# Kernel optimization log

Hardware: AMD Instinct MI355X
Metric: run time of the kernel (lower is better)

## Reference

```python
import jax, jax.numpy as jnp
import numpy as np

B, F, W, H, D = 128, 1024, 32, 64, 64  # batch, n_features, window_size, hidden_state, output_dim


def setup_inputs() -> dict:
    key = jax.random.key(0)
    ks = jax.random.split(key, 8)
    sd = 0.05
    return {
        "x": jax.random.normal(ks[0], (B, F, W), jnp.float32),
        # dense_state: Dense(output_dim) on concat([cell, hidden]) -> [2H, D]
        "W_state": jax.random.normal(ks[1], (2 * H, D), jnp.float32) * sd,
        "b_state": jnp.zeros((D,), jnp.float32),
        # dense: Dense(output_dim, use_bias=False) on input last dim W -> [W, D]
        "W_in": jax.random.normal(ks[2], (W, D), jnp.float32) * sd,
        # Dense(1) scoring layer (shared; original re-creates it each call)
        "w_attn": jax.random.normal(ks[3], (D, 1), jnp.float32) * sd,
        "b_attn": jnp.zeros((1,), jnp.float32),
        # Keras LSTMCell params, gate order i, f, g(c~), o
        "Wx": jax.random.normal(ks[4], (F, 4 * H), jnp.float32) * sd,
        "Wh": jax.random.normal(ks[5], (H, 4 * H), jnp.float32) * sd,
        "b_lstm": jnp.zeros((4 * H,), jnp.float32),
    }


def _forward(x, W_state, b_state, W_in, w_attn, b_attn, Wx, Wh, b_lstm):
    b, f, w = x.shape
    h_dim = Wh.shape[0]
    # dense(input) is loop-invariant: [B, F, D]
    dense_in = jnp.einsum('bfw,wd->bfd', x, W_in)
    xs = jnp.moveaxis(x, 2, 0)  # [W, B, F]: per-timestep slices input[:, :, i]
    h0 = jnp.zeros((b, h_dim), x.dtype)
    c0 = jnp.zeros((b, h_dim), x.dtype)

    def step(carry, x_t):
        h, c = carry
        # original unpacks `s, h = state` with state=[h,c], so it concats [cell, hidden]
        attn_in = jnp.concatenate([c, h], axis=1)             # [B, 2H]
        z = jnp.tanh(attn_in @ W_state + b_state)[:, None, :] + dense_in  # [B, F, D]
        presoft = z @ w_attn + b_attn                         # [B, F, 1]
        # faithful: softmax over last (size-1) axis -> all ones
        alpha = jax.nn.softmax(presoft, axis=-1)
        x_tilde = alpha[..., 0] * x_t                         # [B, F]
        gates = x_tilde @ Wx + h @ Wh + b_lstm                # [B, 4H]
        i_g, f_g, g_g, o_g = jnp.split(gates, 4, axis=1)
        c_new = jax.nn.sigmoid(f_g) * c + jax.nn.sigmoid(i_g) * jnp.tanh(g_g)
        h_new = jax.nn.sigmoid(o_g) * jnp.tanh(c_new)
        # original appends state[1] == CELL state (due to the s,h swap)
        return (h_new, c_new), c_new

    _, outs = jax.lax.scan(step, (h0, c0), xs)                # [W, B, H]
    return jnp.transpose(outs, (1, 0, 2))                     # [B, W, H]


def reference(x, W_state, b_state, W_in, w_attn, b_attn, Wx, Wh, b_lstm):
    return _forward(x, W_state, b_state, W_in, w_attn, b_attn, Wx, Wh, b_lstm)
```

## Files before the change

### kernel.cpp

```cpp
#include <hip/hip_runtime.h>
#include <math.h>

#define B_   128
#define F_   1024
#define W_   32
#define H_   64
#define K4H  256
#define M_   (B_ * W_)
#define K2_  (2 * F_)

typedef __attribute__((ext_vector_type(8))) short  short8;
typedef __attribute__((ext_vector_type(4))) float  f32x4;

__device__ __forceinline__ unsigned bf16_rne(float v) {
  unsigned u = __float_as_uint(v);
  return (u + 0x7FFFu + ((u >> 16) & 1u)) >> 16;
}
__device__ __forceinline__ unsigned pack_hilo(float v) {
  unsigned hi = bf16_rne(v);
  float    hf = __uint_as_float(hi << 16);
  unsigned lo = bf16_rne(v - hf);
  return hi | (lo << 16);
}

__global__ __launch_bounds__(256) void conv_w(const float* __restrict__ Wx,
                                              unsigned* __restrict__ B2) {
  __shared__ unsigned T[256][17];
  const int tid = threadIdx.x;
  const int f0  = blockIdx.x * 16;
#pragma unroll
  for (int i = 0; i < 4; ++i) {
    int l = tid + i * 256;
    int n0 = (l & 63) * 4;
    int fl = l >> 6;
    float4 v = *(const float4*)&Wx[(size_t)(f0 + fl) * K4H + n0];
    T[n0 + 0][fl] = pack_hilo(v.x);
    T[n0 + 1][fl] = pack_hilo(v.y);
    T[n0 + 2][fl] = pack_hilo(v.z);
    T[n0 + 3][fl] = pack_hilo(v.w);
  }
  __syncthreads();
#pragma unroll
  for (int i = 0; i < 4; ++i) {
    int l  = tid + i * 256;
    int c4 = (l & 3) * 4;
    int n  = l >> 2;
    uint4 o;
    o.x = T[n][c4 + 0]; o.y = T[n][c4 + 1]; o.z = T[n][c4 + 2]; o.w = T[n][c4 + 3];
    *(uint4*)&B2[(size_t)n * (K2_ / 2) + f0 + c4] = o;
  }
}

template <int S>
__global__ __launch_bounds__(256, 1) void gemm_mfma(
    const float* __restrict__ x,
    const unsigned* __restrict__ B2,
    float* __restrict__ Gp) {
  constexpr int NIT = 32 / S;
  __shared__ unsigned lA[128 * 36];
  __shared__ unsigned lB[128 * 36];
  const int tid   = threadIdx.x;
  const int mtile = blockIdx.x;
  const int ntile = blockIdx.y;
  const int s     = blockIdx.z;
  const int wv = tid >> 6, lane = tid & 63;
  const int wm = wv & 1, wn = wv >> 1;
  const int lm = lane & 15, q = lane >> 4;

  f32x4 acc[4][4];
#pragma unroll
  for (int a = 0; a < 4; ++a)
#pragma unroll
    for (int bb = 0; bb < 4; ++bb) acc[a][bb] = (f32x4){0.f, 0.f, 0.f, 0.f};

  const int b0 = mtile * 4;
  float4 ax[4];
  uint4  bxr[4];

  auto prefetch = [&](int iter) {
    const int f0 = (s * NIT + iter) * 32;
#pragma unroll
    for (int i = 0; i < 4; ++i) {
      int l  = tid + i * 256;
      int t0 = (l & 7) * 4;
      int fl = (l >> 3) & 31;
      int bl = l >> 8;
      ax[i] = *(const float4*)&x[(((size_t)(b0 + bl)) * F_ + (f0 + fl)) * W_ + t0];
    }
#pragma unroll
    for (int i = 0; i < 4; ++i) {
      int l   = tid + i * 256;
      int c16 = l & 7;
      int nl  = l >> 3;
      bxr[i] = *(const uint4*)&B2[(size_t)(ntile * 128 + nl) * (K2_ / 2) + f0 + c16 * 4];
    }
  };

  prefetch(0);
  const int jx = (tid >> 3) & 3;
  for (int iter = 0; iter < NIT; ++iter) {
    __syncthreads();
#pragma unroll
    for (int i = 0; i < 4; ++i) {
      int l  = tid + i * 256;
      int t0 = (l & 7) * 4;
      int fl = (l >> 3) & 31;
      int bl = l >> 8;
      int m0 = bl * 32 + t0;
      float vals[4] = {ax[i].x, ax[i].y, ax[i].z, ax[i].w};
#pragma unroll
      for (int j = 0; j < 4; ++j) {
        int jj = j ^ jx;
        lA[(m0 + jj) * 36 + fl] = pack_hilo(vals[jj]);
      }
    }
#pragma unroll
    for (int i = 0; i < 4; ++i) {
      int l   = tid + i * 256;
      int c16 = l & 7;
      int nl  = l >> 3;
      *(uint4*)&lB[nl * 36 + c16 * 4] = bxr[i];
    }
    __syncthreads();
    if (iter + 1 < NIT) prefetch(iter + 1);
#pragma unroll
    for (int step = 0; step < 2; ++step) {
      short8 aF[4], bF[4];
#pragma unroll
      for (int mt = 0; mt < 4; ++mt) {
        int row = wm * 64 + mt * 16 + lm;
        aF[mt] = *(const short8*)&lA[row * 36 + step * 16 + q * 4];
      }
#pragma unroll
      for (int nt = 0; nt < 4; ++nt) {
        int row = wn * 64 + nt * 16 + lm;
        bF[nt] = *(const short8*)&lB[row * 36 + step * 16 + q * 4];
      }
#pragma unroll
      for (int mt = 0; mt < 4; ++mt)
#pragma unroll
        for (int nt = 0; nt < 4; ++nt)
          acc[mt][nt] = __builtin_amdgcn_mfma_f32_16x16x32_bf16(
              aF[mt], bF[nt], acc[mt][nt], 0, 0, 0);
    }
  }
  float* Gs = Gp + (size_t)s * ((size_t)M_ * K4H);
#pragma unroll
  for (int mt = 0; mt < 4; ++mt)
#pragma unroll
    for (int nt = 0; nt < 4; ++nt)
#pragma unroll
      for (int r = 0; r < 4; ++r) {
        int m = mtile * 128 + wm * 64 + mt * 16 + q * 4 + r;
        int n = ntile * 128 + wn * 64 + nt * 16 + lm;
        Gs[(size_t)m * K4H + n] = acc[mt][nt][r];
      }
}

__device__ __forceinline__ float bcastlane(float v, int l) {
  return __uint_as_float(__builtin_amdgcn_readlane(__float_as_uint(v), l));
}
__device__ __forceinline__ float sigm(float v)   { return 1.f / (1.f + __expf(-v)); }
__device__ __forceinline__ float tanh_f(float v) { return 1.f - 2.f / (__expf(2.f * v) + 1.f); }

template <int S>
__global__ __launch_bounds__(256, 1) void lstm_seq(
    const float* __restrict__ Gp, const float* __restrict__ Wh,
    const float* __restrict__ bl, float* __restrict__ out) {
  __shared__ float sact[2][4][64];
  const int b = blockIdx.x, tid = threadIdx.x;
  const int w = tid >> 6, u = tid & 63;
  const int k = w * 64 + u;

  float wc[64];
#pragma unroll
  for (int j = 0; j < 64; ++j) wc[j] = Wh[j * K4H + k];
  const float bk = bl[k];
  const size_t base = (size_t)b * W_ * K4H + k;
  const size_t sstr = (size_t)M_ * K4H;

  float h = 0.f, c = 0.f;
  float p = 0.f;
#pragma unroll
  for (int ss = 0; ss < S; ++ss) p += Gp[ss * sstr + base];

  for (int t = 0; t < W_; ++t) {
    float nx = 0.f;
    if (t + 1 < W_) {
#pragma unroll
      for (int ss = 0; ss < S; ++ss)
        nx += Gp[ss * sstr + base + (size_t)(t + 1) * K4H];
    }
    float a0 = p + bk, a1 = 0.f, a2 = 0.f, a3 = 0.f;
#pragma unroll
    for (int j = 0; j < 64; j += 4) {
      a0 = fmaf(bcastlane(h, j),     wc[j],     a0);
      a1 = fmaf(bcastlane(h, j + 1), wc[j + 1], a1);
      a2 = fmaf(bcastlane(h, j + 2), wc[j + 2], a2);
      a3 = fmaf(bcastlane(h, j + 3), wc[j + 3], a3);
    }
    float g = (a0 + a1) + (a2 + a3);
    float act = (w == 2) ? tanh_f(g) : sigm(g);
    sact[t & 1][w][u] = act;
    __syncthreads();
    float si = sact[t & 1][0][u];
    float sf = sact[t & 1][1][u];
    float tg = sact[t & 1][2][u];
    float so = sact[t & 1][3][u];
    c = fmaf(sf, c, si * tg);
    h = so * tanh_f(c);
    if (w == 0) out[((size_t)b * W_ + t) * H_ + u] = c;
    p = nx;
  }
}

extern "C" void kernel_launch(void* const* d_in, const int* in_sizes, int n_in,
                              void* d_out, int out_size, void* d_ws, size_t ws_size,
                              hipStream_t stream) {
  const float* x      = (const float*)d_in[0];
  const float* Wx     = (const float*)d_in[6];
  const float* Wh     = (const float*)d_in[7];
  const float* b_lstm = (const float*)d_in[8];
  float* out = (float*)d_out;

  const size_t gbytes = (size_t)M_ * K4H * sizeof(float);

  if (ws_size >= 4 * gbytes + (1u << 20)) {
    float*    Gp = (float*)d_ws;
    unsigned* B2 = (unsigned*)((char*)d_ws + 4 * gbytes);
    conv_w      <<<dim3(64),       dim3(256), 0, stream>>>(Wx, B2);
    gemm_mfma<4><<<dim3(32, 2, 4), dim3(256), 0, stream>>>(x, B2, Gp);
    lstm_seq<4> <<<dim3(B_),       dim3(256), 0, stream>>>(Gp, Wh, b_lstm, out);
  } else if (ws_size >= 2 * gbytes + (1u << 20)) {
    float*    Gp = (float*)d_ws;
    unsigned* B2 = (unsigned*)((char*)d_ws + 2 * gbytes);
    conv_w      <<<dim3(64),       dim3(256), 0, stream>>>(Wx, B2);
    gemm_mfma<2><<<dim3(32, 2, 2), dim3(256), 0, stream>>>(x, B2, Gp);
    lstm_seq<2> <<<dim3(B_),       dim3(256), 0, stream>>>(Gp, Wh, b_lstm, out);
  } else {
    float*    Gp = (float*)d_ws;
    unsigned* B2 = (unsigned*)((char*)d_ws + gbytes);
    conv_w      <<<dim3(64),       dim3(256), 0, stream>>>(Wx, B2);
    gemm_mfma<1><<<dim3(32, 2, 1), dim3(256), 0, stream>>>(x, B2, Gp);
    lstm_seq<1> <<<dim3(B_),       dim3(256), 0, stream>>>(Gp, Wh, b_lstm, out);
  }
}
```

Before: 119.6 us.

## Fuse input-projection GEMM into per-batch LSTM kernel via shared memory

Replaces the split-K GEMM kernel plus separate LSTM kernel with one kernel per batch row. Each block computes that row's 32x256 input-gate preactivations with MFMA, keeps them in LDS, then runs the recurrence. This removes the global round trip of the gate buffer, the split-K partial sums and one launch. In exchange each block streams the whole converted Wx (1 MB, read by all 128 blocks) and has less GEMM parallelism per block.

```diff
diff --git a/kernel.cpp b/kernel.cpp
--- a/kernel.cpp
+++ b/kernel.cpp
@@ -6,8 +6,8 @@
 #define W_   32
 #define H_   64
 #define K4H  256
-#define M_   (B_ * W_)
 #define K2_  (2 * F_)
+#define KU_  (K2_ / 2)
 
 typedef __attribute__((ext_vector_type(8))) short  short8;
 typedef __attribute__((ext_vector_type(4))) float  f32x4;
@@ -47,114 +47,8 @@
     int n  = l >> 2;
     uint4 o;
     o.x = T[n][c4 + 0]; o.y = T[n][c4 + 1]; o.z = T[n][c4 + 2]; o.w = T[n][c4 + 3];
-    *(uint4*)&B2[(size_t)n * (K2_ / 2) + f0 + c4] = o;
+    *(uint4*)&B2[(size_t)n * KU_ + f0 + c4] = o;
   }
-}
-
-template <int S>
-__global__ __launch_bounds__(256, 1) void gemm_mfma(
-    const float* __restrict__ x,
-    const unsigned* __restrict__ B2,
-    float* __restrict__ Gp) {
-  constexpr int NIT = 32 / S;
-  __shared__ unsigned lA[128 * 36];
-  __shared__ unsigned lB[128 * 36];
-  const int tid   = threadIdx.x;
-  const int mtile = blockIdx.x;
-  const int ntile = blockIdx.y;
-  const int s     = blockIdx.z;
-  const int wv = tid >> 6, lane = tid & 63;
-  const int wm = wv & 1, wn = wv >> 1;
-  const int lm = lane & 15, q = lane >> 4;
-
-  f32x4 acc[4][4];
-#pragma unroll
-  for (int a = 0; a < 4; ++a)
-#pragma unroll
-    for (int bb = 0; bb < 4; ++bb) acc[a][bb] = (f32x4){0.f, 0.f, 0.f, 0.f};
-
-  const int b0 = mtile * 4;
-  float4 ax[4];
-  uint4  bxr[4];
-
-  auto prefetch = [&](int iter) {
-    const int f0 = (s * NIT + iter) * 32;
-#pragma unroll
-    for (int i = 0; i < 4; ++i) {
-      int l  = tid + i * 256;
-      int t0 = (l & 7) * 4;
-      int fl = (l >> 3) & 31;
-      int bl = l >> 8;
-      ax[i] = *(const float4*)&x[(((size_t)(b0 + bl)) * F_ + (f0 + fl)) * W_ + t0];
-    }
-#pragma unroll
-    for (int i = 0; i < 4; ++i) {
-      int l   = tid + i * 256;
-      int c16 = l & 7;
-      int nl  = l >> 3;
-      bxr[i] = *(const uint4*)&B2[(size_t)(ntile * 128 + nl) * (K2_ / 2) + f0 + c16 * 4];
-    }
-  };
-
-  prefetch(0);
-  const int jx = (tid >> 3) & 3;
-  for (int iter = 0; iter < NIT; ++iter) {
-    __syncthreads();
-#pragma unroll
-    for (int i = 0; i < 4; ++i) {
-      int l  = tid + i * 256;
-      int t0 = (l & 7) * 4;
-      int fl = (l >> 3) & 31;
-      int bl = l >> 8;
-      int m0 = bl * 32 + t0;
-      float vals[4] = {ax[i].x, ax[i].y, ax[i].z, ax[i].w};
-#pragma unroll
-      for (int j = 0; j < 4; ++j) {
-        int jj = j ^ jx;
-        lA[(m0 + jj) * 36 + fl] = pack_hilo(vals[jj]);
-      }
-    }
-#pragma unroll
-    for (int i = 0; i < 4; ++i) {
-      int l   = tid + i * 256;
-      int c16 = l & 7;
-      int nl  = l >> 3;
-      *(uint4*)&lB[nl * 36 + c16 * 4] = bxr[i];
-    }
-    __syncthreads();
-    if (iter + 1 < NIT) prefetch(iter + 1);
-#pragma unroll
-    for (int step = 0; step < 2; ++step) {
-      short8 aF[4], bF[4];
-#pragma unroll
-      for (int mt = 0; mt < 4; ++mt) {
-        int row = wm * 64 + mt * 16 + lm;
-        aF[mt] = *(const short8*)&lA[row * 36 + step * 16 + q * 4];
-      }
-#pragma unroll
-      for (int nt = 0; nt < 4; ++nt) {
-        int row = wn * 64 + nt * 16 + lm;
-        bF[nt] = *(const short8*)&lB[row * 36 + step * 16 + q * 4];
-      }
-#pragma unroll
-      for (int mt = 0; mt < 4; ++mt)
-#pragma unroll
-        for (int nt = 0; nt < 4; ++nt)
-          acc[mt][nt] = __builtin_amdgcn_mfma_f32_16x16x32_bf16(
-              aF[mt], bF[nt], acc[mt][nt], 0, 0, 0);
-    }
-  }
-  float* Gs = Gp + (size_t)s * ((size_t)M_ * K4H);
-#pragma unroll
-  for (int mt = 0; mt < 4; ++mt)
-#pragma unroll
-    for (int nt = 0; nt < 4; ++nt)
-#pragma unroll
-      for (int r = 0; r < 4; ++r) {
-        int m = mtile * 128 + wm * 64 + mt * 16 + q * 4 + r;
-        int n = ntile * 128 + wn * 64 + nt * 16 + lm;
-        Gs[(size_t)m * K4H + n] = acc[mt][nt][r];
-      }
 }
 
 __device__ __forceinline__ float bcastlane(float v, int l) {
@@ -163,35 +57,103 @@
 __device__ __forceinline__ float sigm(float v)   { return 1.f / (1.f + __expf(-v)); }
 __device__ __forceinline__ float tanh_f(float v) { return 1.f - 2.f / (__expf(2.f * v) + 1.f); }
 
-template <int S>
-__global__ __launch_bounds__(256, 1) void lstm_seq(
-    const float* __restrict__ Gp, const float* __restrict__ Wh,
-    const float* __restrict__ bl, float* __restrict__ out) {
-  __shared__ float sact[2][4][64];
-  const int b = blockIdx.x, tid = threadIdx.x;
-  const int w = tid >> 6, u = tid & 63;
-  const int k = w * 64 + u;
+__global__ __launch_bounds__(256, 1) void fused_rnn(
+    const float* __restrict__ x,
+    const unsigned* __restrict__ B2,
+    const float* __restrict__ Wh,
+    const float* __restrict__ bl,
+    float* __restrict__ out) {
+  __shared__ unsigned lA[32 * 36];
+  __shared__ unsigned lB[256 * 36];
+  __shared__ float    sG[32][260];
+  __shared__ float    sact[2][4][64];
 
+  const int tid  = threadIdx.x;
+  const int b    = blockIdx.x;
+  const int wv   = tid >> 6, lane = tid & 63;
+  const int lm   = lane & 15, q = lane >> 4;
+
+  f32x4 acc[2][4];
+#pragma unroll
+  for (int a = 0; a < 2; ++a)
+#pragma unroll
+    for (int bb = 0; bb < 4; ++bb) acc[a][bb] = (f32x4){0.f, 0.f, 0.f, 0.f};
+
+  const int t0 = (tid & 7) * 4;
+  const int fl = tid >> 3;
+  const int jx = (tid >> 3) & 3;
+
+  float4 ax;
+  uint4  bxr[8];
+
+  auto prefetch = [&](int iter) {
+    const int f0 = iter * 32;
+    ax = *(const float4*)&x[((size_t)b * F_ + (f0 + fl)) * W_ + t0];
+#pragma unroll
+    for (int i = 0; i < 8; ++i) {
+      int l   = tid + i * 256;
+      int c16 = l & 7;
+      int nl  = l >> 3;
+      bxr[i] = *(const uint4*)&B2[(size_t)nl * KU_ + f0 + c16 * 4];
+    }
+  };
+
+  prefetch(0);
+  for (int iter = 0; iter < 32; ++iter) {
+    __syncthreads();
+    {
+      float vals[4] = {ax.x, ax.y, ax.z, ax.w};
+#pragma unroll
+      for (int j = 0; j < 4; ++j) {
+        int jj = j ^ jx;
+        lA[(t0 + jj) * 36 + fl] = pack_hilo(vals[jj]);
+      }
+    }
+#pragma unroll
+    for (int i = 0; i < 8; ++i) {
+      int l   = tid + i * 256;
+      int c16 = l & 7;
+      int nl  = l >> 3;
+      *(uint4*)&lB[nl * 36 + c16 * 4] = bxr[i];
+    }
+    __syncthreads();
+    if (iter + 1 < 32) prefetch(iter + 1);
+#pragma unroll
+    for (int step = 0; step < 2; ++step) {
+      short8 aF[2], bF[4];
+#pragma unroll
+      for (int mt = 0; mt < 2; ++mt)
+        aF[mt] = *(const short8*)&lA[(mt * 16 + lm) * 36 + step * 16 + q * 4];
+#pragma unroll
+      for (int nt = 0; nt < 4; ++nt)
+        bF[nt] = *(const short8*)&lB[(wv * 64 + nt * 16 + lm) * 36 + step * 16 + q * 4];
+#pragma unroll
+      for (int mt = 0; mt < 2; ++mt)
+#pragma unroll
+        for (int nt = 0; nt < 4; ++nt)
+          acc[mt][nt] = __builtin_amdgcn_mfma_f32_16x16x32_bf16(
+              aF[mt], bF[nt], acc[mt][nt], 0, 0, 0);
+    }
+  }
+
+  const int k = wv * 64 + lane;
   float wc[64];
 #pragma unroll
   for (int j = 0; j < 64; ++j) wc[j] = Wh[j * K4H + k];
   const float bk = bl[k];
-  const size_t base = (size_t)b * W_ * K4H + k;
-  const size_t sstr = (size_t)M_ * K4H;
+
+#pragma unroll
+  for (int mt = 0; mt < 2; ++mt)
+#pragma unroll
+    for (int nt = 0; nt < 4; ++nt)
+#pragma unroll
+      for (int r = 0; r < 4; ++r)
+        sG[mt * 16 + q * 4 + r][wv * 64 + nt * 16 + lm] = acc[mt][nt][r];
+  __syncthreads();
 
   float h = 0.f, c = 0.f;
-  float p = 0.f;
-#pragma unroll
-  for (int ss = 0; ss < S; ++ss) p += Gp[ss * sstr + base];
-
   for (int t = 0; t < W_; ++t) {
-    float nx = 0.f;
-    if (t + 1 < W_) {
-#pragma unroll
-      for (int ss = 0; ss < S; ++ss)
-        nx += Gp[ss * sstr + base + (size_t)(t + 1) * K4H];
-    }
-    float a0 = p + bk, a1 = 0.f, a2 = 0.f, a3 = 0.f;
+    float a0 = sG[t][k] + bk, a1 = 0.f, a2 = 0.f, a3 = 0.f;
 #pragma unroll
     for (int j = 0; j < 64; j += 4) {
       a0 = fmaf(bcastlane(h, j),     wc[j],     a0);
@@ -200,17 +162,16 @@
       a3 = fmaf(bcastlane(h, j + 3), wc[j + 3], a3);
     }
     float g = (a0 + a1) + (a2 + a3);
-    float act = (w == 2) ? tanh_f(g) : sigm(g);
-    sact[t & 1][w][u] = act;
+    float act = (wv == 2) ? tanh_f(g) : sigm(g);
+    sact[t & 1][wv][lane] = act;
     __syncthreads();
-    float si = sact[t & 1][0][u];
-    float sf = sact[t & 1][1][u];
-    float tg = sact[t & 1][2][u];
-    float so = sact[t & 1][3][u];
+    float si = sact[t & 1][0][lane];
+    float sf = sact[t & 1][1][lane];
+    float tg = sact[t & 1][2][lane];
+    float so = sact[t & 1][3][lane];
     c = fmaf(sf, c, si * tg);
     h = so * tanh_f(c);
-    if (w == 0) out[((size_t)b * W_ + t) * H_ + u] = c;
-    p = nx;
+    if (wv == 0) out[((size_t)b * W_ + t) * H_ + lane] = c;
   }
 }
 
@@ -223,25 +184,8 @@
   const float* b_lstm = (const float*)d_in[8];
   float* out = (float*)d_out;
 
-  const size_t gbytes = (size_t)M_ * K4H * sizeof(float);
+  unsigned* B2 = (unsigned*)d_ws;
 
-  if (ws_size >= 4 * gbytes + (1u << 20)) {
-    float*    Gp = (float*)d_ws;
-    unsigned* B2 = (unsigned*)((char*)d_ws + 4 * gbytes);
-    conv_w      <<<dim3(64),       dim3(256), 0, stream>>>(Wx, B2);
-    gemm_mfma<4><<<dim3(32, 2, 4), dim3(256), 0, stream>>>(x, B2, Gp);
-    lstm_seq<4> <<<dim3(B_),       dim3(256), 0, stream>>>(Gp, Wh, b_lstm, out);
-  } else if (ws_size >= 2 * gbytes + (1u << 20)) {
-    float*    Gp = (float*)d_ws;
-    unsigned* B2 = (unsigned*)((char*)d_ws + 2 * gbytes);
-    conv_w      <<<dim3(64),       dim3(256), 0, stream>>>(Wx, B2);
-    gemm_mfma<2><<<dim3(32, 2, 2), dim3(256), 0, stream>>>(x, B2, Gp);
-    lstm_seq<2> <<<dim3(B_),       dim3(256), 0, stream>>>(Gp, Wh, b_lstm, out);
-  } else {
-    float*    Gp = (float*)d_ws;
-    unsigned* B2 = (unsigned*)((char*)d_ws + gbytes);
-    conv_w      <<<dim3(64),       dim3(256), 0, stream>>>(Wx, B2);
-    gemm_mfma<1><<<dim3(32, 2, 1), dim3(256), 0, stream>>>(x, B2, Gp);
-    lstm_seq<1> <<<dim3(B_),       dim3(256), 0, stream>>>(Gp, Wh, b_lstm, out);
-  }
+  conv_w   <<<dim3(64), dim3(256), 0, stream>>>(Wx, B2);
+  fused_rnn<<<dim3(B_), dim3(256), 0, stream>>>(x, B2, Wh, b_lstm, out);
 }
```

Result: slower. 178.8 us (+49.5%).

## Run LSTM recurrence in a single wavefront per batch row, removing block barriers

Applied to the files above, without the earlier changes.

The sequential LSTM kernel changes from four waves (one per gate) that exchange activations through shared memory with a __syncthreads each timestep to a single 64-lane wave per batch row. Each lane now holds all four gate weight columns (256 registers) and computes every gate itself. This removes the per-step LDS round trip and barrier on the serial critical path, but each wave now does four times the FMA work per step and carries heavy register pressure, which may cause spills.

```diff
diff --git a/kernel.cpp b/kernel.cpp
--- a/kernel.cpp
+++ b/kernel.cpp
@@ -164,53 +164,58 @@
 __device__ __forceinline__ float tanh_f(float v) { return 1.f - 2.f / (__expf(2.f * v) + 1.f); }
 
 template <int S>
-__global__ __launch_bounds__(256, 1) void lstm_seq(
+__global__ __launch_bounds__(64, 1) void lstm_wave(
     const float* __restrict__ Gp, const float* __restrict__ Wh,
     const float* __restrict__ bl, float* __restrict__ out) {
-  __shared__ float sact[2][4][64];
-  const int b = blockIdx.x, tid = threadIdx.x;
-  const int w = tid >> 6, u = tid & 63;
-  const int k = w * 64 + u;
-
-  float wc[64];
-#pragma unroll
-  for (int j = 0; j < 64; ++j) wc[j] = Wh[j * K4H + k];
-  const float bk = bl[k];
-  const size_t base = (size_t)b * W_ * K4H + k;
+  const int b = blockIdx.x;
+  const int u = threadIdx.x;
+
+  float wI[64], wF[64], wG[64], wO[64];
+#pragma unroll
+  for (int j = 0; j < 64; ++j) {
+    const float* r = &Wh[(size_t)j * K4H + u];
+    wI[j] = r[0]; wF[j] = r[64]; wG[j] = r[128]; wO[j] = r[192];
+  }
+  const float bI = bl[u], bF_ = bl[64 + u], bG = bl[128 + u], bO = bl[192 + u];
+
+  const float* Gb  = Gp + (size_t)b * W_ * K4H + u;
   const size_t sstr = (size_t)M_ * K4H;
 
+  float pf[4 * S];
+#pragma unroll
+  for (int ss = 0; ss < S; ++ss)
+#pragma unroll
+    for (int g = 0; g < 4; ++g)
+      pf[ss * 4 + g] = Gb[(size_t)ss * sstr + g * 64];
+
   float h = 0.f, c = 0.f;
-  float p = 0.f;
-#pragma unroll
-  for (int ss = 0; ss < S; ++ss) p += Gp[ss * sstr + base];
-
+#pragma unroll 1
   for (int t = 0; t < W_; ++t) {
-    float nx = 0.f;
+    float aI = bI, aF = bF_, aG = bG, aO = bO;
+#pragma unroll
+    for (int ss = 0; ss < S; ++ss) {
+      aI += pf[ss * 4 + 0]; aF += pf[ss * 4 + 1];
+      aG += pf[ss * 4 + 2]; aO += pf[ss * 4 + 3];
+    }
     if (t + 1 < W_) {
+      const float* Gn = Gb + (size_t)(t + 1) * K4H;
 #pragma unroll
       for (int ss = 0; ss < S; ++ss)
-        nx += Gp[ss * sstr + base + (size_t)(t + 1) * K4H];
-    }
-    float a0 = p + bk, a1 = 0.f, a2 = 0.f, a3 = 0.f;
-#pragma unroll
-    for (int j = 0; j < 64; j += 4) {
-      a0 = fmaf(bcastlane(h, j),     wc[j],     a0);
-      a1 = fmaf(bcastlane(h, j + 1), wc[j + 1], a1);
-      a2 = fmaf(bcastlane(h, j + 2), wc[j + 2], a2);
-      a3 = fmaf(bcastlane(h, j + 3), wc[j + 3], a3);
-    }
-    float g = (a0 + a1) + (a2 + a3);
-    float act = (w == 2) ? tanh_f(g) : sigm(g);
-    sact[t & 1][w][u] = act;
-    __syncthreads();
-    float si = sact[t & 1][0][u];
-    float sf = sact[t & 1][1][u];
-    float tg = sact[t & 1][2][u];
-    float so = sact[t & 1][3][u];
-    c = fmaf(sf, c, si * tg);
-    h = so * tanh_f(c);
-    if (w == 0) out[((size_t)b * W_ + t) * H_ + u] = c;
-    p = nx;
+#pragma unroll
+        for (int g = 0; g < 4; ++g)
+          pf[ss * 4 + g] = Gn[(size_t)ss * sstr + g * 64];
+    }
+#pragma unroll
+    for (int j = 0; j < 64; ++j) {
+      float hj = bcastlane(h, j);
+      aI = fmaf(hj, wI[j], aI);
+      aF = fmaf(hj, wF[j], aF);
+      aG = fmaf(hj, wG[j], aG);
+      aO = fmaf(hj, wO[j], aO);
+    }
+    c = fmaf(sigm(aF), c, sigm(aI) * tanh_f(aG));
+    h = sigm(aO) * tanh_f(c);
+    out[((size_t)b * W_ + t) * H_ + u] = c;
   }
 }
 
@@ -230,18 +235,18 @@
     unsigned* B2 = (unsigned*)((char*)d_ws + 4 * gbytes);
     conv_w      <<<dim3(64),       dim3(256), 0, stream>>>(Wx, B2);
     gemm_mfma<4><<<dim3(32, 2, 4), dim3(256), 0, stream>>>(x, B2, Gp);
-    lstm_seq<4> <<<dim3(B_),       dim3(256), 0, stream>>>(Gp, Wh, b_lstm, out);
+    lstm_wave<4><<<dim3(B_),       dim3(64),  0, stream>>>(Gp, Wh, b_lstm, out);
   } else if (ws_size >= 2 * gbytes + (1u << 20)) {
     float*    Gp = (float*)d_ws;
     unsigned* B2 = (unsigned*)((char*)d_ws + 2 * gbytes);
     conv_w      <<<dim3(64),       dim3(256), 0, stream>>>(Wx, B2);
     gemm_mfma<2><<<dim3(32, 2, 2), dim3(256), 0, stream>>>(x, B2, Gp);
-    lstm_seq<2> <<<dim3(B_),       dim3(256), 0, stream>>>(Gp, Wh, b_lstm, out);
+    lstm_wave<2><<<dim3(B_),       dim3(64),  0, stream>>>(Gp, Wh, b_lstm, out);
   } else {
     float*    Gp = (float*)d_ws;
     unsigned* B2 = (unsigned*)((char*)d_ws + gbytes);
     conv_w      <<<dim3(64),       dim3(256), 0, stream>>>(Wx, B2);
     gemm_mfma<1><<<dim3(32, 2, 1), dim3(256), 0, stream>>>(x, B2, Gp);
-    lstm_seq<1> <<<dim3(B_),       dim3(256), 0, stream>>>(Gp, Wh, b_lstm, out);
-  }
-}
+    lstm_wave<1><<<dim3(B_),       dim3(64),  0, stream>>>(Gp, Wh, b_lstm, out);
+  }
+}
```

Measured after the change: 135.3 us. 1.13x slower.
